# Kernel tuning notes

Measured on AMD Instinct MI355X. Metric: run time of the kernel, lower is better.

The kernel has to match this reference:

```python
import jax, jax.numpy as jnp
import numpy as np

B, T, C = 4, 4096, 512
H, KS = 8, 9
D = C // H
PAD = KS // 2


def setup_inputs() -> dict:
    key = jax.random.key(0)
    ks = jax.random.split(key, 9)
    s = 1.0 / np.sqrt(C)
    return {
        "x": jax.random.normal(ks[0], (B, T, C), jnp.float32),
        "Wq": jax.random.normal(ks[1], (C, C), jnp.float32) * s,
        "bq": jax.random.normal(ks[2], (C,), jnp.float32) * 0.01,
        "Wk": jax.random.normal(ks[3], (C, C), jnp.float32) * s,
        "bk": jax.random.normal(ks[4], (C,), jnp.float32) * 0.01,
        "Wv": jax.random.normal(ks[5], (C, C), jnp.float32) * s,
        "bv": jax.random.normal(ks[6], (C,), jnp.float32) * 0.01,
        "Wo": jax.random.normal(ks[7], (C, C), jnp.float32) * s,
        "bo": jax.random.normal(ks[8], (C,), jnp.float32) * 0.01,
    }


def reference(x, Wq, bq, Wk, bk, Wv, bv, Wo, bo):
    Bx, Tx, Cx = x.shape
    # projections (torch Linear: x @ W.T + b), split heads -> (B,H,T,D)
    q = (x @ Wq.T + bq).reshape(Bx, Tx, H, D).transpose(0, 2, 1, 3)
    k = (x @ Wk.T + bk).reshape(Bx, Tx, H, D).transpose(0, 2, 1, 3)
    v = (x @ Wv.T + bv).reshape(Bx, Tx, H, D).transpose(0, 2, 1, 3)
    # replicate-pad along time (matches F.pad mode='replicate')
    k_pad = jnp.pad(k, ((0, 0), (0, 0), (PAD, PAD), (0, 0)), mode='edge')
    v_pad = jnp.pad(v, ((0, 0), (0, 0), (PAD, PAD), (0, 0)), mode='edge')
    # window gather indices: (T, KS) into padded time axis
    idx = jnp.arange(Tx)[:, None] + jnp.arange(KS)[None, :]
    k_unf = k_pad[:, :, idx, :]  # (B,H,T,KS,D)
    v_unf = v_pad[:, :, idx, :]  # (B,H,T,KS,D)
    scale = 1.0 / np.sqrt(D)
    scores = jnp.einsum('bhtd,bhtkd->bhtk', q, k_unf) * scale  # (B,H,T,KS)
    attn = jax.nn.softmax(scores, axis=-1)
    y = jnp.einsum('bhtk,bhtkd->bhtd', attn, v_unf)  # (B,H,T,D)
    y = y.transpose(0, 2, 1, 3).reshape(Bx, Tx, Cx)
    return y @ Wo.T + bo
```

## Files before the change

### kernel.cpp

```cpp
#include <hip/hip_runtime.h>
#include <hip/hip_bf16.h>

#define B_    4
#define T_    4096
#define C_    512
#define H_    8
#define D_    64
#define KS_   9
#define PAD_  4
#define MTOT  (B_ * T_)
#define PLANE (MTOT * C_)
#define XU    (MTOT * C_ / 8)
#define WU    (C_ * C_ / 8)

typedef __bf16 bf16_t;
typedef __bf16 bf16x8 __attribute__((ext_vector_type(8)));
typedef float  f32x4  __attribute__((ext_vector_type(4)));

__global__ __launch_bounds__(256)
void conv_all(const float* __restrict__ x,  const float* __restrict__ Wq,
              const float* __restrict__ Wk, const float* __restrict__ Wv,
              const float* __restrict__ Wo, bf16_t* __restrict__ dst) {
  int i = blockIdx.x * 256 + threadIdx.x;
  const float* s;
  if (i < XU) {
    s = x + (size_t)i * 8;
  } else {
    int r = i - XU;
    int w = r >> 15;
    const float* W = (w == 0) ? Wq : (w == 1) ? Wk : (w == 2) ? Wv : Wo;
    s = W + (size_t)(r & (WU - 1)) * 8;
  }
  float4 f0 = ((const float4*)s)[0];
  float4 f1 = ((const float4*)s)[1];
  bf16x8 o;
  o[0] = (bf16_t)f0.x; o[1] = (bf16_t)f0.y; o[2] = (bf16_t)f0.z; o[3] = (bf16_t)f0.w;
  o[4] = (bf16_t)f1.x; o[5] = (bf16_t)f1.y; o[6] = (bf16_t)f1.z; o[7] = (bf16_t)f1.w;
  ((bf16x8*)dst)[i] = o;
}

template <bool APLANE>
__device__ __forceinline__ void gemm_main(const bf16_t* __restrict__ A,
                                          const bf16_t* __restrict__ W,
                                          int m0, int n0, f32x4 acc[4][4]) {
  constexpr int K = C_;
  __shared__ __align__(16) bf16_t lsA[128 * 64];
  __shared__ __align__(16) bf16_t lsB[128 * 64];

  const int tid  = threadIdx.x;
  const int lane = tid & 63;
  const int wave = tid >> 6;
  const int wm   = (wave >> 1) * 64;
  const int wn   = (wave & 1) * 64;

  for (int k0 = 0; k0 < K; k0 += 64) {
    __syncthreads();
#pragma unroll
    for (int s = 0; s < 4; ++s) {
      int u    = s * 256 + tid;
      int row  = u >> 3;
      int slot = u & 7;
      int c    = slot ^ (row & 7);
      const bf16_t* ga;
      if (APLANE) {
        int m = m0 + row;
        int b = m >> 12, t = m & (T_ - 1);
        int h = k0 >> 6;
        ga = A + (((size_t)(b * H_ + h) * T_ + t) * D_ + c * 8);
      } else {
        ga = A + ((size_t)(m0 + row) * K + k0 + c * 8);
      }
      const bf16_t* gb = W + ((size_t)(n0 + row) * K + k0 + c * 8);
      __builtin_amdgcn_global_load_lds(
          (const __attribute__((address_space(1))) unsigned int*)ga,
          (__attribute__((address_space(3))) unsigned int*)&lsA[u * 8], 16, 0, 0);
      __builtin_amdgcn_global_load_lds(
          (const __attribute__((address_space(1))) unsigned int*)gb,
          (__attribute__((address_space(3))) unsigned int*)&lsB[u * 8], 16, 0, 0);
    }
    __syncthreads();

    const int rr = lane & 15;
    const int q  = lane >> 4;
#pragma unroll
    for (int kh = 0; kh < 2; ++kh) {
      const int cg = kh * 4 + q;
      const int sl = (cg ^ (rr & 7)) << 3;
      bf16x8 af[4], bfr[4];
#pragma unroll
      for (int i = 0; i < 4; ++i) {
        af[i]  = *(const bf16x8*)&lsA[(wm + i * 16 + rr) * 64 + sl];
        bfr[i] = *(const bf16x8*)&lsB[(wn + i * 16 + rr) * 64 + sl];
      }
#pragma unroll
      for (int i = 0; i < 4; ++i)
#pragma unroll
        for (int j = 0; j < 4; ++j)
          acc[i][j] = __builtin_amdgcn_mfma_f32_16x16x32_bf16(
              af[i], bfr[j], acc[i][j], 0, 0, 0);
    }
  }
}

__global__ __launch_bounds__(256, 2)
void qkv_gemm(const bf16_t* __restrict__ xb, const bf16_t* __restrict__ Wb,
              const float* __restrict__ bq, const float* __restrict__ bk,
              const float* __restrict__ bv, bf16_t* __restrict__ qkv) {
  const int z  = blockIdx.z;
  const int m0 = blockIdx.y * 128, n0 = blockIdx.x * 128;
  f32x4 acc[4][4] = {};
  gemm_main<false>(xb, Wb + (size_t)z * C_ * C_, m0, n0, acc);

  const float* bias = (z == 0) ? bq : (z == 1) ? bk : bv;
  const int tid = threadIdx.x, lane = tid & 63, wave = tid >> 6;
  const int wm = (wave >> 1) * 64, wn = (wave & 1) * 64;
  const int cn = lane & 15, rb = (lane >> 4) << 2;

  float bvals[4];
#pragma unroll
  for (int j = 0; j < 4; ++j) bvals[j] = bias[n0 + wn + j * 16 + cn];

  const int bb = m0 >> 12;
  const int hh = (n0 + wn) >> 6;
  bf16_t* hb = qkv + (size_t)z * PLANE + (size_t)(bb * H_ + hh) * T_ * D_;
#pragma unroll
  for (int i = 0; i < 4; ++i) {
#pragma unroll
    for (int r = 0; r < 4; ++r) {
      int t = (m0 + wm + i * 16 + rb + r) & (T_ - 1);
      bf16_t* row = hb + (size_t)t * D_;
#pragma unroll
      for (int j = 0; j < 4; ++j)
        row[j * 16 + cn] = (bf16_t)(acc[i][j][r] + bvals[j]);
    }
  }
}

__global__ __launch_bounds__(256, 2)
void out_gemm(const bf16_t* __restrict__ y, const bf16_t* __restrict__ Wob,
              const float* __restrict__ bo, float* __restrict__ out) {
  const int m0 = blockIdx.y * 128, n0 = blockIdx.x * 128;
  f32x4 acc[4][4] = {};
  gemm_main<true>(y, Wob, m0, n0, acc);

  const int tid = threadIdx.x, lane = tid & 63, wave = tid >> 6;
  const int wm = (wave >> 1) * 64, wn = (wave & 1) * 64;
  const int cn = lane & 15, rb = (lane >> 4) << 2;
  float bvals[4];
#pragma unroll
  for (int j = 0; j < 4; ++j) bvals[j] = bo[n0 + wn + j * 16 + cn];
#pragma unroll
  for (int i = 0; i < 4; ++i) {
#pragma unroll
    for (int r = 0; r < 4; ++r) {
      int gm = m0 + wm + i * 16 + rb + r;
      float* orow = out + (size_t)gm * C_ + (n0 + wn);
#pragma unroll
      for (int j = 0; j < 4; ++j)
        orow[j * 16 + cn] = acc[i][j][r] + bvals[j];
    }
  }
}

__global__ __launch_bounds__(256)
void attn_kernel(const bf16_t* __restrict__ qkv, bf16_t* __restrict__ y) {
  const int tid  = threadIdx.x;
  const int sub  = tid & 7;
  const int tl   = tid >> 3;
  const int t    = blockIdx.x * 32 + tl;
  const int h    = blockIdx.y;
  const int b    = blockIdx.z;

  const size_t pl = (size_t)(b * H_ + h) * T_ * D_;
  const bf16_t* q = qkv + pl;
  const bf16_t* k = qkv + (size_t)PLANE + pl;
  const bf16_t* v = qkv + (size_t)2 * PLANE + pl;
  const int c = sub * 8;

  int tj[KS_];
#pragma unroll
  for (int j = 0; j < KS_; ++j) {
    int tt = t - PAD_ + j;
    tj[j] = tt < 0 ? 0 : (tt >= T_ ? T_ - 1 : tt);
  }

  bf16x8 q8 = *(const bf16x8*)(q + (size_t)t * D_ + c);
  float qf[8];
#pragma unroll
  for (int e = 0; e < 8; ++e) qf[e] = (float)q8[e];

  float s[KS_];
#pragma unroll
  for (int j = 0; j < KS_; ++j) {
    bf16x8 k8 = *(const bf16x8*)(k + (size_t)tj[j] * D_ + c);
    float d0 = 0.f;
#pragma unroll
    for (int e = 0; e < 8; ++e) d0 += qf[e] * (float)k8[e];
    s[j] = d0;
  }

#pragma unroll
  for (int m = 1; m < 8; m <<= 1)
#pragma unroll
    for (int j = 0; j < KS_; ++j) s[j] += __shfl_xor(s[j], m, 8);

  float mx = s[0];
#pragma unroll
  for (int j = 1; j < KS_; ++j) mx = fmaxf(mx, s[j]);
  float w[KS_], sum = 0.f;
#pragma unroll
  for (int j = 0; j < KS_; ++j) {
    w[j] = __expf((s[j] - mx) * 0.125f);
    sum += w[j];
  }
  const float inv = 1.f / sum;
#pragma unroll
  for (int j = 0; j < KS_; ++j) w[j] *= inv;

  float o[8] = {0.f, 0.f, 0.f, 0.f, 0.f, 0.f, 0.f, 0.f};
#pragma unroll
  for (int j = 0; j < KS_; ++j) {
    bf16x8 v8 = *(const bf16x8*)(v + (size_t)tj[j] * D_ + c);
#pragma unroll
    for (int e = 0; e < 8; ++e) o[e] += w[j] * (float)v8[e];
  }
  bf16x8 o8;
#pragma unroll
  for (int e = 0; e < 8; ++e) o8[e] = (bf16_t)o[e];
  *(bf16x8*)(y + pl + (size_t)t * D_ + c) = o8;
}

extern "C" void kernel_launch(void* const* d_in, const int* in_sizes, int n_in,
                              void* d_out, int out_size, void* d_ws, size_t ws_size,
                              hipStream_t stream) {
  const float* x  = (const float*)d_in[0];
  const float* Wq = (const float*)d_in[1];
  const float* bq = (const float*)d_in[2];
  const float* Wk = (const float*)d_in[3];
  const float* bk = (const float*)d_in[4];
  const float* Wv = (const float*)d_in[5];
  const float* bv = (const float*)d_in[6];
  const float* Wo = (const float*)d_in[7];
  const float* bo = (const float*)d_in[8];
  float* out = (float*)d_out;

  bf16_t* xb  = (bf16_t*)d_ws;
  bf16_t* Wb  = xb + (size_t)MTOT * C_;
  bf16_t* qkv = Wb + (size_t)4 * C_ * C_;
  bf16_t* y   = qkv + (size_t)3 * PLANE;

  conv_all<<<(XU + 4 * WU) / 256, 256, 0, stream>>>(x, Wq, Wk, Wv, Wo, xb);
  qkv_gemm<<<dim3(C_ / 128, MTOT / 128, 3), 256, 0, stream>>>(
      xb, Wb, bq, bk, bv, qkv);
  attn_kernel<<<dim3(T_ / 32, H_, B_), 256, 0, stream>>>(qkv, y);
  out_gemm<<<dim3(C_ / 128, MTOT / 128, 1), 256, 0, stream>>>(
      y, Wb + (size_t)3 * C_ * C_, bo, out);
}
```

Baseline: 174.1 us.

## Enlarge QKV GEMM tile to 256x128 and stage K/V windows in LDS for attention

The QKV projection now uses 256x128 block tiles, with each wave computing a 64x128 sub-tile (4x8 MFMA accumulators). This raises reuse of each loaded W tile and halves the number of blocks. The attention kernel now handles 128 time steps per block and first copies the padded K/V window (136 rows) into shared memory, so the 9 overlapping neighbour reads hit LDS instead of global memory. The trade-offs are doubled accumulator registers in the GEMM, which may hurt occupancy or spill, and more LDS use plus fewer blocks for attention.

```diff
diff --git a/kernel.cpp b/kernel.cpp
--- a/kernel.cpp
+++ b/kernel.cpp
@@ -39,11 +39,99 @@
   ((bf16x8*)dst)[i] = o;
 }
 
-template <bool APLANE>
-__device__ __forceinline__ void gemm_main(const bf16_t* __restrict__ A,
-                                          const bf16_t* __restrict__ W,
-                                          int m0, int n0, f32x4 acc[4][4]) {
-  constexpr int K = C_;
+__global__ __launch_bounds__(256, 2)
+void qkv_gemm(const bf16_t* __restrict__ xb, const bf16_t* __restrict__ Wb,
+              const float* __restrict__ bq, const float* __restrict__ bk,
+              const float* __restrict__ bv, bf16_t* __restrict__ qkv) {
+  __shared__ __align__(16) bf16_t lsA[256 * 64];
+  __shared__ __align__(16) bf16_t lsB[128 * 64];
+
+  const int z    = blockIdx.z;
+  const int m0   = blockIdx.y * 256;
+  const int n0   = blockIdx.x * 128;
+  const bf16_t* W = Wb + (size_t)z * C_ * C_;
+
+  const int tid  = threadIdx.x;
+  const int lane = tid & 63;
+  const int wave = tid >> 6;
+  const int wm   = wave * 64;
+
+  f32x4 acc[4][8] = {};
+
+  for (int k0 = 0; k0 < C_; k0 += 64) {
+    __syncthreads();
+#pragma unroll
+    for (int s = 0; s < 8; ++s) {
+      int u    = s * 256 + tid;
+      int row  = u >> 3;
+      int c    = (u & 7) ^ (row & 7);
+      const bf16_t* ga = xb + ((size_t)(m0 + row) * C_ + k0 + c * 8);
+      __builtin_amdgcn_global_load_lds(
+          (const __attribute__((address_space(1))) unsigned int*)ga,
+          (__attribute__((address_space(3))) unsigned int*)&lsA[u * 8], 16, 0, 0);
+    }
+#pragma unroll
+    for (int s = 0; s < 4; ++s) {
+      int u    = s * 256 + tid;
+      int row  = u >> 3;
+      int c    = (u & 7) ^ (row & 7);
+      const bf16_t* gb = W + ((size_t)(n0 + row) * C_ + k0 + c * 8);
+      __builtin_amdgcn_global_load_lds(
+          (const __attribute__((address_space(1))) unsigned int*)gb,
+          (__attribute__((address_space(3))) unsigned int*)&lsB[u * 8], 16, 0, 0);
+    }
+    __syncthreads();
+
+    const int rr = lane & 15;
+    const int q  = lane >> 4;
+#pragma unroll
+    for (int kh = 0; kh < 2; ++kh) {
+      const int cg = kh * 4 + q;
+      const int sl = (cg ^ (rr & 7)) << 3;
+      bf16x8 af[4], bfr[8];
+#pragma unroll
+      for (int i = 0; i < 4; ++i)
+        af[i] = *(const bf16x8*)&lsA[(wm + i * 16 + rr) * 64 + sl];
+#pragma unroll
+      for (int j = 0; j < 8; ++j)
+        bfr[j] = *(const bf16x8*)&lsB[(j * 16 + rr) * 64 + sl];
+#pragma unroll
+      for (int i = 0; i < 4; ++i)
+#pragma unroll
+        for (int j = 0; j < 8; ++j)
+          acc[i][j] = __builtin_amdgcn_mfma_f32_16x16x32_bf16(
+              af[i], bfr[j], acc[i][j], 0, 0, 0);
+    }
+  }
+
+  const int cn = lane & 15;
+  const int rb = (lane >> 4) << 2;
+  const float* bias = (z == 0) ? bq : (z == 1) ? bk : bv;
+  float bvals[8];
+#pragma unroll
+  for (int j = 0; j < 8; ++j) bvals[j] = bias[n0 + j * 16 + cn];
+
+  bf16_t* plz = qkv + (size_t)z * PLANE;
+#pragma unroll
+  for (int i = 0; i < 4; ++i) {
+#pragma unroll
+    for (int r = 0; r < 4; ++r) {
+      int m  = m0 + wm + i * 16 + rb + r;
+      int bb = m >> 12, t = m & (T_ - 1);
+#pragma unroll
+      for (int j = 0; j < 8; ++j) {
+        int col = n0 + j * 16 + cn;
+        int h = col >> 6, d = col & 63;
+        plz[((size_t)(bb * H_ + h) * T_ + t) * D_ + d] =
+            (bf16_t)(acc[i][j][r] + bvals[j]);
+      }
+    }
+  }
+}
+
+__global__ __launch_bounds__(256, 2)
+void out_gemm(const bf16_t* __restrict__ y, const bf16_t* __restrict__ Wob,
+              const float* __restrict__ bo, float* __restrict__ out) {
   __shared__ __align__(16) bf16_t lsA[128 * 64];
   __shared__ __align__(16) bf16_t lsB[128 * 64];
 
@@ -52,25 +140,23 @@
   const int wave = tid >> 6;
   const int wm   = (wave >> 1) * 64;
   const int wn   = (wave & 1) * 64;
-
-  for (int k0 = 0; k0 < K; k0 += 64) {
+  const int m0   = blockIdx.y * 128;
+  const int n0   = blockIdx.x * 128;
+
+  f32x4 acc[4][4] = {};
+
+  for (int k0 = 0; k0 < C_; k0 += 64) {
     __syncthreads();
 #pragma unroll
     for (int s = 0; s < 4; ++s) {
       int u    = s * 256 + tid;
       int row  = u >> 3;
-      int slot = u & 7;
-      int c    = slot ^ (row & 7);
-      const bf16_t* ga;
-      if (APLANE) {
-        int m = m0 + row;
-        int b = m >> 12, t = m & (T_ - 1);
-        int h = k0 >> 6;
-        ga = A + (((size_t)(b * H_ + h) * T_ + t) * D_ + c * 8);
-      } else {
-        ga = A + ((size_t)(m0 + row) * K + k0 + c * 8);
-      }
-      const bf16_t* gb = W + ((size_t)(n0 + row) * K + k0 + c * 8);
+      int c    = (u & 7) ^ (row & 7);
+      int m = m0 + row;
+      int b = m >> 12, t = m & (T_ - 1);
+      int h = k0 >> 6;
+      const bf16_t* ga = y + (((size_t)(b * H_ + h) * T_ + t) * D_ + c * 8);
+      const bf16_t* gb = Wob + ((size_t)(n0 + row) * C_ + k0 + c * 8);
       __builtin_amdgcn_global_load_lds(
           (const __attribute__((address_space(1))) unsigned int*)ga,
           (__attribute__((address_space(3))) unsigned int*)&lsA[u * 8], 16, 0, 0);
@@ -100,52 +186,9 @@
               af[i], bfr[j], acc[i][j], 0, 0, 0);
     }
   }
-}
-
-__global__ __launch_bounds__(256, 2)
-void qkv_gemm(const bf16_t* __restrict__ xb, const bf16_t* __restrict__ Wb,
-              const float* __restrict__ bq, const float* __restrict__ bk,
-              const float* __restrict__ bv, bf16_t* __restrict__ qkv) {
-  const int z  = blockIdx.z;
-  const int m0 = blockIdx.y * 128, n0 = blockIdx.x * 128;
-  f32x4 acc[4][4] = {};
-  gemm_main<false>(xb, Wb + (size_t)z * C_ * C_, m0, n0, acc);
-
-  const float* bias = (z == 0) ? bq : (z == 1) ? bk : bv;
-  const int tid = threadIdx.x, lane = tid & 63, wave = tid >> 6;
-  const int wm = (wave >> 1) * 64, wn = (wave & 1) * 64;
-  const int cn = lane & 15, rb = (lane >> 4) << 2;
-
-  float bvals[4];
-#pragma unroll
-  for (int j = 0; j < 4; ++j) bvals[j] = bias[n0 + wn + j * 16 + cn];
-
-  const int bb = m0 >> 12;
-  const int hh = (n0 + wn) >> 6;
-  bf16_t* hb = qkv + (size_t)z * PLANE + (size_t)(bb * H_ + hh) * T_ * D_;
-#pragma unroll
-  for (int i = 0; i < 4; ++i) {
-#pragma unroll
-    for (int r = 0; r < 4; ++r) {
-      int t = (m0 + wm + i * 16 + rb + r) & (T_ - 1);
-      bf16_t* row = hb + (size_t)t * D_;
-#pragma unroll
-      for (int j = 0; j < 4; ++j)
-        row[j * 16 + cn] = (bf16_t)(acc[i][j][r] + bvals[j]);
-    }
-  }
-}
-
-__global__ __launch_bounds__(256, 2)
-void out_gemm(const bf16_t* __restrict__ y, const bf16_t* __restrict__ Wob,
-              const float* __restrict__ bo, float* __restrict__ out) {
-  const int m0 = blockIdx.y * 128, n0 = blockIdx.x * 128;
-  f32x4 acc[4][4] = {};
-  gemm_main<true>(y, Wob, m0, n0, acc);
-
-  const int tid = threadIdx.x, lane = tid & 63, wave = tid >> 6;
-  const int wm = (wave >> 1) * 64, wn = (wave & 1) * 64;
-  const int cn = lane & 15, rb = (lane >> 4) << 2;
+
+  const int cn = lane & 15;
+  const int rb = (lane >> 4) << 2;
   float bvals[4];
 #pragma unroll
   for (int j = 0; j < 4; ++j) bvals[j] = bo[n0 + wn + j * 16 + cn];
@@ -162,72 +205,85 @@
   }
 }
 
+#define AT_T 128
+#define AT_R (AT_T + 8)
 __global__ __launch_bounds__(256)
 void attn_kernel(const bf16_t* __restrict__ qkv, bf16_t* __restrict__ y) {
-  const int tid  = threadIdx.x;
-  const int sub  = tid & 7;
-  const int tl   = tid >> 3;
-  const int t    = blockIdx.x * 32 + tl;
-  const int h    = blockIdx.y;
-  const int b    = blockIdx.z;
+  __shared__ __align__(16) bf16_t ks[AT_R * D_];
+  __shared__ __align__(16) bf16_t vs[AT_R * D_];
+
+  const int tid = threadIdx.x;
+  const int t0  = blockIdx.x * AT_T;
+  const int h   = blockIdx.y;
+  const int b   = blockIdx.z;
 
   const size_t pl = (size_t)(b * H_ + h) * T_ * D_;
-  const bf16_t* q = qkv + pl;
-  const bf16_t* k = qkv + (size_t)PLANE + pl;
-  const bf16_t* v = qkv + (size_t)2 * PLANE + pl;
-  const int c = sub * 8;
-
-  int tj[KS_];
-#pragma unroll
-  for (int j = 0; j < KS_; ++j) {
-    int tt = t - PAD_ + j;
-    tj[j] = tt < 0 ? 0 : (tt >= T_ ? T_ - 1 : tt);
-  }
-
-  bf16x8 q8 = *(const bf16x8*)(q + (size_t)t * D_ + c);
-  float qf[8];
-#pragma unroll
-  for (int e = 0; e < 8; ++e) qf[e] = (float)q8[e];
-
-  float s[KS_];
-#pragma unroll
-  for (int j = 0; j < KS_; ++j) {
-    bf16x8 k8 = *(const bf16x8*)(k + (size_t)tj[j] * D_ + c);
-    float d0 = 0.f;
-#pragma unroll
-    for (int e = 0; e < 8; ++e) d0 += qf[e] * (float)k8[e];
-    s[j] = d0;
-  }
-
-#pragma unroll
-  for (int m = 1; m < 8; m <<= 1)
-#pragma unroll
-    for (int j = 0; j < KS_; ++j) s[j] += __shfl_xor(s[j], m, 8);
-
-  float mx = s[0];
-#pragma unroll
-  for (int j = 1; j < KS_; ++j) mx = fmaxf(mx, s[j]);
-  float w[KS_], sum = 0.f;
-#pragma unroll
-  for (int j = 0; j < KS_; ++j) {
-    w[j] = __expf((s[j] - mx) * 0.125f);
-    sum += w[j];
-  }
-  const float inv = 1.f / sum;
-#pragma unroll
-  for (int j = 0; j < KS_; ++j) w[j] *= inv;
-
-  float o[8] = {0.f, 0.f, 0.f, 0.f, 0.f, 0.f, 0.f, 0.f};
-#pragma unroll
-  for (int j = 0; j < KS_; ++j) {
-    bf16x8 v8 = *(const bf16x8*)(v + (size_t)tj[j] * D_ + c);
-#pragma unroll
-    for (int e = 0; e < 8; ++e) o[e] += w[j] * (float)v8[e];
-  }
-  bf16x8 o8;
-#pragma unroll
-  for (int e = 0; e < 8; ++e) o8[e] = (bf16_t)o[e];
-  *(bf16x8*)(y + pl + (size_t)t * D_ + c) = o8;
+  const bf16_t* kg = qkv + (size_t)PLANE + pl;
+  const bf16_t* vg = qkv + (size_t)2 * PLANE + pl;
+
+  for (int c = tid; c < AT_R * 8; c += 256) {
+    int r = c >> 3, off = (c & 7) * 8;
+    int tg = t0 - PAD_ + r;
+    tg = tg < 0 ? 0 : (tg >= T_ ? T_ - 1 : tg);
+    *((bf16x8*)ks + c) = *(const bf16x8*)(kg + (size_t)tg * D_ + off);
+    *((bf16x8*)vs + c) = *(const bf16x8*)(vg + (size_t)tg * D_ + off);
+  }
+  __syncthreads();
+
+  const int sub = tid & 7;
+  const int tl  = tid >> 3;
+  const int c8  = sub * 8;
+
+#pragma unroll
+  for (int p = 0; p < AT_T / 32; ++p) {
+    const int tloc = p * 32 + tl;
+    const int t    = t0 + tloc;
+
+    bf16x8 q8 = *(const bf16x8*)(qkv + pl + (size_t)t * D_ + c8);
+    float qf[8];
+#pragma unroll
+    for (int e = 0; e < 8; ++e) qf[e] = (float)q8[e];
+
+    float s[KS_];
+#pragma unroll
+    for (int j = 0; j < KS_; ++j) {
+      bf16x8 k8 = *(const bf16x8*)&ks[(tloc + j) * D_ + c8];
+      float d0 = 0.f;
+#pragma unroll
+      for (int e = 0; e < 8; ++e) d0 += qf[e] * (float)k8[e];
+      s[j] = d0;
+    }
+
+#pragma unroll
+    for (int m = 1; m < 8; m <<= 1)
+#pragma unroll
+      for (int j = 0; j < KS_; ++j) s[j] += __shfl_xor(s[j], m, 8);
+
+    float mx = s[0];
+#pragma unroll
+    for (int j = 1; j < KS_; ++j) mx = fmaxf(mx, s[j]);
+    float w[KS_], sum = 0.f;
+#pragma unroll
+    for (int j = 0; j < KS_; ++j) {
+      w[j] = __expf((s[j] - mx) * 0.125f);
+      sum += w[j];
+    }
+    const float inv = 1.f / sum;
+#pragma unroll
+    for (int j = 0; j < KS_; ++j) w[j] *= inv;
+
+    float o[8] = {0.f, 0.f, 0.f, 0.f, 0.f, 0.f, 0.f, 0.f};
+#pragma unroll
+    for (int j = 0; j < KS_; ++j) {
+      bf16x8 v8 = *(const bf16x8*)&vs[(tloc + j) * D_ + c8];
+#pragma unroll
+      for (int e = 0; e < 8; ++e) o[e] += w[j] * (float)v8[e];
+    }
+    bf16x8 o8;
+#pragma unroll
+    for (int e = 0; e < 8; ++e) o8[e] = (bf16_t)o[e];
+    *(bf16x8*)(y + pl + (size_t)t * D_ + c8) = o8;
+  }
 }
 
 extern "C" void kernel_launch(void* const* d_in, const int* in_sizes, int n_in,
@@ -250,9 +306,9 @@
   bf16_t* y   = qkv + (size_t)3 * PLANE;
 
   conv_all<<<(XU + 4 * WU) / 256, 256, 0, stream>>>(x, Wq, Wk, Wv, Wo, xb);
-  qkv_gemm<<<dim3(C_ / 128, MTOT / 128, 3), 256, 0, stream>>>(
+  qkv_gemm<<<dim3(C_ / 128, MTOT / 256, 3), 256, 0, stream>>>(
       xb, Wb, bq, bk, bv, qkv);
-  attn_kernel<<<dim3(T_ / 32, H_, B_), 256, 0, stream>>>(qkv, y);
+  attn_kernel<<<dim3(T_ / AT_T, H_, B_), 256, 0, stream>>>(qkv, y);
   out_gemm<<<dim3(C_ / 128, MTOT / 128, 1), 256, 0, stream>>>(
       y, Wb + (size_t)3 * C_ * C_, bo, out);
 }
```

Result: no change. 171.3 us (-1.6%).
